# Performance work log

Measured on AMD Instinct MI355X. Metric: run time of the kernel, lower is better.

Reference implementation:

```python
import jax, jax.numpy as jnp
import numpy as np

N_HEAD = 16


def setup_inputs() -> dict:
    key = jax.random.key(0)
    k1, k2, k3 = jax.random.split(key, 3)
    B, T, C = 4, 2048, 2048
    x = jax.random.normal(k1, (B, T, C), dtype=jnp.float32)
    # weights stored as [in, out] so y = x @ W + b (equivalent to torch Linear)
    w_attn = jax.random.normal(k2, (C, 3 * C), dtype=jnp.float32) * 0.02
    b_attn = jnp.zeros((3 * C,), dtype=jnp.float32)
    w_proj = jax.random.normal(k3, (C, C), dtype=jnp.float32) * 0.02
    b_proj = jnp.zeros((C,), dtype=jnp.float32)
    return {"x": x, "w_attn": w_attn, "b_attn": b_attn, "w_proj": w_proj, "b_proj": b_proj}


def reference(x, w_attn, b_attn, w_proj, b_proj):
    B, T, C = x.shape
    H = N_HEAD
    D = C // H
    qkv = x @ w_attn + b_attn                     # [B,T,3C]
    q, k, v = jnp.split(qkv, 3, axis=-1)
    q = q.reshape(B, T, H, D).transpose(0, 2, 1, 3)  # [B,H,T,D]
    k = k.reshape(B, T, H, D).transpose(0, 2, 1, 3)
    v = v.reshape(B, T, H, D).transpose(0, 2, 1, 3)
    att = jnp.einsum("bhqd,bhkd->bhqk", q, k) * (1.0 / jnp.sqrt(jnp.float32(D)))
    causal = jnp.tril(jnp.ones((T, T), dtype=bool))
    att = jnp.where(causal[None, None], att, jnp.float32(-jnp.inf))
    att = jax.nn.softmax(att, axis=-1)
    y = jnp.einsum("bhqk,bhkd->bhqd", att, v)     # [B,H,T,D]
    y = y.transpose(0, 2, 1, 3).reshape(B, T, C)
    return y @ w_proj + b_proj
```

## Files before the change

### kernel.cpp

```cpp
#include <hip/hip_runtime.h>
#include <cstdint>

typedef unsigned short u16;
typedef u16   u16x4 __attribute__((ext_vector_type(4)));
typedef u16   u16x8 __attribute__((ext_vector_type(8)));
typedef short s16x8 __attribute__((ext_vector_type(8)));
typedef float f32x4 __attribute__((ext_vector_type(4)));

__device__ __forceinline__ u16 f2bf(float f) {
  union { float f; unsigned u; } v; v.f = f;
  unsigned u = v.u;
  return (u16)((u + 0x7fffu + ((u >> 16) & 1u)) >> 16);
}

__device__ __forceinline__ void gld_lds16(const u16* g, u16* l) {
  __builtin_amdgcn_global_load_lds((const __attribute__((address_space(1))) void*)g,
                                   (__attribute__((address_space(3))) void*)l, 16, 0, 0);
}

__device__ __forceinline__ void transpose_cast_body(
    const float* __restrict__ in, u16* __restrict__ outp, int R, int Cin,
    int cx, int cy, u16 (*tile)[72]) {
  const int c0 = cx * 64, r0 = cy * 64;
  const int t = threadIdx.x;
  const int r = t >> 2, cs = (t & 3) * 16;
  const float* src = in + (size_t)(r0 + r) * Cin + c0 + cs;
#pragma unroll
  for (int q = 0; q < 4; ++q) {
    float4 v = *(const float4*)(src + q * 4);
    tile[r][cs + q * 4 + 0] = f2bf(v.x);
    tile[r][cs + q * 4 + 1] = f2bf(v.y);
    tile[r][cs + q * 4 + 2] = f2bf(v.z);
    tile[r][cs + q * 4 + 3] = f2bf(v.w);
  }
  __syncthreads();
  u16x8 w0, w1;
#pragma unroll
  for (int q = 0; q < 8; ++q) { w0[q] = tile[cs + q][r]; w1[q] = tile[cs + 8 + q][r]; }
  u16* dst = outp + (size_t)(c0 + r) * R + r0 + cs;
  *(u16x8*)dst = w0;
  *(u16x8*)(dst + 8) = w1;
}

__global__ void prep_k(const float* __restrict__ x, u16* __restrict__ xb,
                       const float* __restrict__ w_attn, u16* __restrict__ waT,
                       const float* __restrict__ w_proj, u16* __restrict__ wpT) {
  __shared__ u16 tile[64][72];
  const int bx = blockIdx.x;
  if (bx < 8192) {
    size_t i = ((size_t)bx * 256 + threadIdx.x) * 8;
    float4 a = *(const float4*)(x + i);
    float4 b = *(const float4*)(x + i + 4);
    u16x8 r;
    r[0] = f2bf(a.x); r[1] = f2bf(a.y); r[2] = f2bf(a.z); r[3] = f2bf(a.w);
    r[4] = f2bf(b.x); r[5] = f2bf(b.y); r[6] = f2bf(b.z); r[7] = f2bf(b.w);
    *(u16x8*)(xb + i) = r;
  } else if (bx < 11264) {
    int idx = bx - 8192;
    transpose_cast_body(w_attn, waT, 2048, 6144, idx % 96, idx / 96, tile);
  } else {
    int idx = bx - 11264;
    transpose_cast_body(w_proj, wpT, 2048, 2048, idx % 32, idx / 32, tile);
  }
}

template <int EPI>
__global__ __launch_bounds__(512, 2) void gemm256(
    const u16* __restrict__ A, const u16* __restrict__ Bt,
    const float* __restrict__ bias,
    u16* __restrict__ o0, u16* __restrict__ o1, u16* __restrict__ o2,
    float* __restrict__ ofp, int Ntiles, int Kdim) {
  __shared__ __align__(128) u16 sm[65536];
  const int nwg = gridDim.x;
  const int orig = blockIdx.x;
  const int qq = nwg >> 3;
  const int bid = (orig & 7) * qq + (orig >> 3);
  const int mt = bid / Ntiles, nt = bid % Ntiles;
  const int tid = threadIdx.x, lane = tid & 63, wave = tid >> 6;
  const int wr = wave >> 2, wc = wave & 3;
  const int l15 = lane & 15, lhi = lane >> 4;
  f32x4 acc[8][4] = {};
  const int nK = Kdim >> 6;

#define VMA(n) asm volatile("s_waitcnt vmcnt(" #n ")" ::: "memory")
#define BARK   asm volatile("s_barrier" ::: "memory")
#define DSA(qm)                                                                          \
  do {                                                                                   \
    _Pragma("unroll") for (int mi = 0; mi < 4; ++mi)                                     \
    _Pragma("unroll") for (int kk = 0; kk < 2; ++kk)                                     \
      af[mi * 2 + kk] = *(const s16x8*)&sm[(size_t)(cA + (qm) * 1024 +                   \
          (kk * 4 + lhi) * 128 + wr * 64 + mi * 16 + l15) * 8];                          \
  } while (0)
#define DSB(dst, qn)                                                                     \
  do {                                                                                   \
    _Pragma("unroll") for (int ni = 0; ni < 2; ++ni)                                     \
    _Pragma("unroll") for (int kk = 0; kk < 2; ++kk)                                     \
      dst[ni * 2 + kk] = *(const s16x8*)&sm[(size_t)(cB + (qn) * 1024 +                  \
          (kk * 4 + lhi) * 128 + wc * 32 + ni * 16 + l15) * 8];                          \
  } while (0)
#define STA(qm, k0, sbase)                                                               \
  do {                                                                                   \
    _Pragma("unroll") for (int l = 0; l < 2; ++l)                                        \
      gld_lds16(A + (size_t)(mt * 256 + (wave & 1) * 128 + (qm) * 64 + lane) * Kdim +    \
                    (k0) + (l * 4 + (wave >> 1)) * 8,                                    \
                &sm[(size_t)((sbase) + (qm) * 1024 + l * 512 + wave * 64) * 8]);         \
  } while (0)
#define STB(qn, k0, sbase)                                                               \
  do {                                                                                   \
    _Pragma("unroll") for (int l = 0; l < 2; ++l)                                        \
      gld_lds16(Bt + (size_t)(nt * 256 + ((wave & 1) * 2 + (lane >> 5)) * 64 +           \
                              (qn) * 32 + (lane & 31)) * Kdim +                          \
                     (k0) + (l * 4 + (wave >> 1)) * 8,                                   \
                &sm[(size_t)((sbase) + (qn) * 1024 + l * 512 + wave * 64) * 8]);         \
  } while (0)
#define MM(qm, qn, BF)                                                                   \
  do {                                                                                   \
    __builtin_amdgcn_s_setprio(1);                                                       \
    _Pragma("unroll") for (int mi = 0; mi < 4; ++mi)                                     \
    _Pragma("unroll") for (int ni = 0; ni < 2; ++ni)                                     \
    _Pragma("unroll") for (int kk = 0; kk < 2; ++kk)                                     \
      acc[(qm) * 4 + mi][(qn) * 2 + ni] = __builtin_amdgcn_mfma_f32_16x16x32_bf16(       \
          af[mi * 2 + kk], BF[ni * 2 + kk], acc[(qm) * 4 + mi][(qn) * 2 + ni], 0, 0, 0); \
    __builtin_amdgcn_s_setprio(0);                                                       \
  } while (0)

  STA(0, 0, 0); STB(0, 0, 4096); STB(1, 0, 4096); STA(1, 0, 0);
  VMA(4);
  BARK;

  for (int t = 0; t < nK; ++t) {
    const int cA = (t & 1) * 2048, cB = 4096 + (t & 1) * 2048;
    const int sA = ((t & 1) ^ 1) * 2048, sB = 4096 + ((t & 1) ^ 1) * 2048;
    const int k1 = (t + 1) << 6;
    const bool st = (t + 1 < nK);
    s16x8 af[8], bf0[4], bf1[4];
    DSA(0); DSB(bf0, 0);
    if (st) { STA(0, k1, sA); VMA(4); } else { VMA(2); }
    BARK; MM(0, 0, bf0); BARK;
    DSB(bf1, 1);
    if (st) { STB(0, k1, sB); VMA(4); } else { VMA(0); }
    BARK; MM(0, 1, bf1); BARK;
    DSA(1);
    if (st) STB(1, k1, sB);
    BARK; MM(1, 1, bf1); BARK;
    if (st) { STA(1, k1, sA); VMA(4); }
    BARK; MM(1, 0, bf0); BARK;
  }
#undef VMA
#undef BARK
#undef DSA
#undef DSB
#undef STA
#undef STB
#undef MM

  const int row0 = mt * 256 + wr * 128;
  const int col0 = nt * 256 + wc * 64;
  float bcol[4];
#pragma unroll
  for (int ni = 0; ni < 4; ++ni) bcol[ni] = bias[col0 + ni * 16 + l15];
  if constexpr (EPI == 0) {
#pragma unroll
    for (int ni = 0; ni < 4; ++ni) {
      int cc = col0 + ni * 16 + l15;
      int which = cc >> 11, h = (cc >> 7) & 15, d = cc & 127;
      if (which == 2) {
#pragma unroll
        for (int mi = 0; mi < 8; ++mi) {
          int t0 = row0 + mi * 16 + lhi * 4;
          int bb = t0 >> 11, tt = t0 & 2047;
          u16x4 w;
#pragma unroll
          for (int j = 0; j < 4; ++j) w[j] = f2bf(acc[mi][ni][j] + bcol[ni]);
          *(u16x4*)&o2[(((size_t)bb * 16 + h) * 128 + d) * 2048 + tt] = w;
        }
      } else {
        u16* o = (which == 0) ? o0 : o1;
#pragma unroll
        for (int mi = 0; mi < 8; ++mi)
#pragma unroll
          for (int j = 0; j < 4; ++j) {
            int row = row0 + mi * 16 + lhi * 4 + j;
            int bb = row >> 11, tt = row & 2047;
            o[(((size_t)bb * 16 + h) * 2048 + tt) * 128 + d] = f2bf(acc[mi][ni][j] + bcol[ni]);
          }
      }
    }
  } else {
#pragma unroll
    for (int mi = 0; mi < 8; ++mi)
#pragma unroll
      for (int j = 0; j < 4; ++j) {
        int row = row0 + mi * 16 + lhi * 4 + j;
#pragma unroll
        for (int ni = 0; ni < 4; ++ni)
          ofp[(size_t)row * 2048 + col0 + ni * 16 + l15] = acc[mi][ni][j] + bcol[ni];
      }
  }
}

__global__ __launch_bounds__(512, 4) void attn_k(
    const u16* __restrict__ Q, const u16* __restrict__ Kg,
    const u16* __restrict__ Vt, u16* __restrict__ Y) {
  __shared__ u16 Ks[8192];
  __shared__ u16 Vs[8192];
  __shared__ u16 Ps[8][16 * 72];
  const int p = blockIdx.x, bh = blockIdx.y;
  const int tid = threadIdx.x, lane = tid & 63, wave = tid >> 6;
  const int l15 = lane & 15, lhi = lane >> 4;
  const size_t bhT = (size_t)bh * 2048;
  const int b = bh >> 4, h = bh & 15;
  const float sc = 0.08838834764831845f * 1.4426950408889634f;

  for (int hf = 0; hf < 2; ++hf) {
    const int qt = hf ? 15 - p : p;
    const int r0 = qt * 128 + wave * 16;
    const int last = 2 * qt + 1;

    s16x8 qf[4];
#pragma unroll
    for (int kk = 0; kk < 4; ++kk)
      qf[kk] = *(const s16x8*)&Q[(bhT + r0 + l15) * 128 + kk * 32 + lhi * 8];

    f32x4 o[8] = {};
    float m_[4], l_[4];
#pragma unroll
    for (int j = 0; j < 4; ++j) { m_[j] = -1e30f; l_[j] = 0.f; }

    __syncthreads();
#pragma unroll
    for (int c = 0; c < 2; ++c) {
      int ci = c * 512 + tid;
      int dhi = ci >> 6, key = ci & 63;
      gld_lds16(Kg + (bhT + key) * 128 + dhi * 8, &Ks[(c * 512 + wave * 64) * 8]);
      int khi = ci >> 7, d = ci & 127;
      gld_lds16(Vt + ((size_t)bh * 128 + d) * 2048 + khi * 8, &Vs[(c * 512 + wave * 64) * 8]);
    }
    __syncthreads();

    for (int it = 0; it <= last; ++it) {
      const int j0 = it * 64;
      const bool have_next = (it < last);
      u16x8 kpre[2], vpre[2];
      if (have_next) {
        const int j1 = j0 + 64;
#pragma unroll
        for (int c = 0; c < 2; ++c) {
          int ci = c * 512 + tid;
          int dhi = ci >> 6, key = ci & 63;
          kpre[c] = *(const u16x8*)&Kg[(bhT + j1 + key) * 128 + dhi * 8];
          int khi = ci >> 7, d = ci & 127;
          vpre[c] = *(const u16x8*)&Vt[((size_t)bh * 128 + d) * 2048 + j1 + khi * 8];
        }
      }

      if (j0 <= r0 + 15) {
        f32x4 s[4] = {};
#pragma unroll
        for (int nc = 0; nc < 4; ++nc)
#pragma unroll
          for (int kk = 0; kk < 4; ++kk) {
            s16x8 kf = *(const s16x8*)&Ks[((kk * 4 + lhi) * 64 + nc * 16 + l15) * 8];
            s[nc] = __builtin_amdgcn_mfma_f32_16x16x32_bf16(qf[kk], kf, s[nc], 0, 0, 0);
          }
        const bool maskt = (j0 + 63 > r0);
        float rmax[4];
#pragma unroll
        for (int j = 0; j < 4; ++j) rmax[j] = -1e30f;
#pragma unroll
        for (int nc = 0; nc < 4; ++nc)
#pragma unroll
          for (int j = 0; j < 4; ++j) {
            float v = s[nc][j] * sc;
            if (maskt && (j0 + nc * 16 + l15) > (r0 + lhi * 4 + j)) v = -1e30f;
            s[nc][j] = v;
            rmax[j] = fmaxf(rmax[j], v);
          }
#pragma unroll
        for (int off = 1; off < 16; off <<= 1)
#pragma unroll
          for (int j = 0; j < 4; ++j) rmax[j] = fmaxf(rmax[j], __shfl_xor(rmax[j], off));

        float al[4], rsum[4];
#pragma unroll
        for (int j = 0; j < 4; ++j) {
          float mn = fmaxf(m_[j], rmax[j]);
          al[j] = exp2f(m_[j] - mn);
          m_[j] = mn;
          rsum[j] = 0.f;
        }
#pragma unroll
        for (int nc = 0; nc < 4; ++nc)
#pragma unroll
          for (int j = 0; j < 4; ++j) {
            float pv = exp2f(s[nc][j] - m_[j]);
            rsum[j] += pv;
            Ps[wave][(lhi * 4 + j) * 72 + nc * 16 + l15] = f2bf(pv);
          }
#pragma unroll
        for (int off = 1; off < 16; off <<= 1)
#pragma unroll
          for (int j = 0; j < 4; ++j) rsum[j] += __shfl_xor(rsum[j], off);
#pragma unroll
        for (int j = 0; j < 4; ++j) l_[j] = l_[j] * al[j] + rsum[j];
#pragma unroll
        for (int di = 0; di < 8; ++di)
#pragma unroll
          for (int j = 0; j < 4; ++j) o[di][j] *= al[j];

#pragma unroll
        for (int kk2 = 0; kk2 < 2; ++kk2) {
          s16x8 pf = *(const s16x8*)&Ps[wave][l15 * 72 + kk2 * 32 + lhi * 8];
#pragma unroll
          for (int di = 0; di < 8; ++di) {
            s16x8 vf = *(const s16x8*)&Vs[((kk2 * 4 + lhi) * 128 + di * 16 + l15) * 8];
            o[di] = __builtin_amdgcn_mfma_f32_16x16x32_bf16(pf, vf, o[di], 0, 0, 0);
          }
        }
      }

      if (have_next) {
        __syncthreads();
#pragma unroll
        for (int c = 0; c < 2; ++c) {
          *(u16x8*)&Ks[(c * 512 + tid) * 8] = kpre[c];
          *(u16x8*)&Vs[(c * 512 + tid) * 8] = vpre[c];
        }
        __syncthreads();
      }
    }

    float rl[4];
#pragma unroll
    for (int j = 0; j < 4; ++j) rl[j] = 1.0f / l_[j];
#pragma unroll
    for (int di = 0; di < 8; ++di)
#pragma unroll
      for (int j = 0; j < 4; ++j) {
        int row = b * 2048 + r0 + lhi * 4 + j;
        int col = h * 128 + di * 16 + l15;
        Y[(size_t)row * 2048 + col] = f2bf(o[di][j] * rl[j]);
      }
  }
}

extern "C" void kernel_launch(void* const* d_in, const int* in_sizes, int n_in,
                              void* d_out, int out_size, void* d_ws, size_t ws_size,
                              hipStream_t stream) {
  const float* x      = (const float*)d_in[0];
  const float* w_attn = (const float*)d_in[1];
  const float* b_attn = (const float*)d_in[2];
  const float* w_proj = (const float*)d_in[3];
  const float* b_proj = (const float*)d_in[4];
  float* out = (float*)d_out;

  char* ws = (char*)d_ws;
  u16* xb  = (u16*)(ws);
  u16* waT = (u16*)(ws + 33554432ull);
  u16* wpT = (u16*)(ws + 58720256ull);
  u16* Qb  = (u16*)(ws + 67108864ull);
  u16* Kb  = (u16*)(ws + 100663296ull);
  u16* Vtb = (u16*)(ws + 167772160ull);
  u16* Yb  = xb;

  prep_k<<<12288, 256, 0, stream>>>(x, xb, w_attn, waT, w_proj, wpT);
  gemm256<0><<<32 * 24, 512, 0, stream>>>(xb, waT, b_attn, Qb, Kb, Vtb, nullptr, 24, 2048);
  attn_k<<<dim3(8, 64), 512, 0, stream>>>(Qb, Kb, Vtb, Yb);
  gemm256<1><<<32 * 8, 512, 0, stream>>>(Yb, wpT, b_proj, nullptr, nullptr, nullptr, out, 8, 2048);
}
```

Measured before the change: 554.6 us.

## Deepen GEMM global-to-LDS prefetch to two K-tiles ahead

Restructures the 256x256 GEMM main loop so global-to-LDS loads are issued up to two K steps ahead instead of one. The quarter-tile LDS slots are reused in a staggered order, and the loop is peeled into a steady state plus two epilogue iterations with adjusted vmcnt wait counts. The aim is to hide more global memory latency behind MFMA work. The cost is more outstanding loads and a tricky buffer-reuse schedule whose correctness depends on the exact wait counts.

Result: no change. 558.0 us (+0.6%).

```diff
diff --git a/kernel.cpp b/kernel.cpp
--- a/kernel.cpp
+++ b/kernel.cpp
@@ -82,7 +82,7 @@
   f32x4 acc[8][4] = {};
   const int nK = Kdim >> 6;
 
-#define VMA(n) asm volatile("s_waitcnt vmcnt(" #n ")" ::: "memory")
+#define VMA(n) asm volatile("s_waitcnt vmcnt(" n ")" ::: "memory")
 #define BARK   asm volatile("s_barrier" ::: "memory")
 #define DSA(qm)                                                                          \
   do {                                                                                   \
@@ -123,29 +123,40 @@
           af[mi * 2 + kk], BF[ni * 2 + kk], acc[(qm) * 4 + mi][(qn) * 2 + ni], 0, 0, 0); \
     __builtin_amdgcn_s_setprio(0);                                                       \
   } while (0)
+#define TILE(t, DO1, DO2, V0, V1, V3)                                                    \
+  do {                                                                                   \
+    const int cA = ((t) & 1) * 2048, cB = 4096 + ((t) & 1) * 2048;                       \
+    const int sA1 = (((t) + 1) & 1) * 2048;                                              \
+    const int sA2 = ((t) & 1) * 2048, sB2 = 4096 + ((t) & 1) * 2048;                     \
+    const int k1 = ((t) + 1) << 6, k2 = ((t) + 2) << 6;                                  \
+    s16x8 af[8], bf0[4], bf1[4];                                                         \
+                                                                                \
+    DSA(0); DSB(bf0, 0);                                                                 \
+    if (DO1) STA(1, k1, sA1);                                                            \
+    VMA(V0); BARK; MM(0, 0, bf0); BARK;                                                  \
+                                                                                \
+    DSB(bf1, 1);                                                                         \
+    if (DO2) STA(0, k2, sA2);                                                            \
+    VMA(V1); BARK; MM(0, 1, bf1); BARK;                                                  \
+                                                                                \
+    DSA(1);                                                                              \
+    if (DO2) STB(0, k2, sB2);                                                            \
+    BARK; MM(1, 1, bf1); BARK;                                                           \
+                                                                                \
+    if (DO2) STB(1, k2, sB2);                                                            \
+    if (DO1) VMA(V3);                                                                    \
+    BARK; MM(1, 0, bf0); BARK;                                                           \
+  } while (0)
 
   STA(0, 0, 0); STB(0, 0, 4096); STB(1, 0, 4096); STA(1, 0, 0);
-  VMA(4);
+  STA(0, 64, 2048); STB(0, 64, 6144); STB(1, 64, 6144);
+  VMA("10");
   BARK;
 
-  for (int t = 0; t < nK; ++t) {
-    const int cA = (t & 1) * 2048, cB = 4096 + (t & 1) * 2048;
-    const int sA = ((t & 1) ^ 1) * 2048, sB = 4096 + ((t & 1) ^ 1) * 2048;
-    const int k1 = (t + 1) << 6;
-    const bool st = (t + 1 < nK);
-    s16x8 af[8], bf0[4], bf1[4];
-    DSA(0); DSB(bf0, 0);
-    if (st) { STA(0, k1, sA); VMA(4); } else { VMA(2); }
-    BARK; MM(0, 0, bf0); BARK;
-    DSB(bf1, 1);
-    if (st) { STB(0, k1, sB); VMA(4); } else { VMA(0); }
-    BARK; MM(0, 1, bf1); BARK;
-    DSA(1);
-    if (st) STB(1, k1, sB);
-    BARK; MM(1, 1, bf1); BARK;
-    if (st) { STA(1, k1, sA); VMA(4); }
-    BARK; MM(1, 0, bf0); BARK;
-  }
+  for (int t = 0; t < nK - 2; ++t) TILE(t, true, true, "10", "10", "10");
+  TILE(nK - 2, true, false, "10", "8", "4");
+  TILE(nK - 1, false, false, "2", "0", "0");
+
 #undef VMA
 #undef BARK
 #undef DSA
@@ -153,6 +164,7 @@
 #undef STA
 #undef STB
 #undef MM
+#undef TILE
 
   const int row0 = mt * 256 + wr * 128;
   const int col0 = nt * 256 + wc * 64;
```

## Restructure GEMM to 256x128 tiles with K=32 triple-buffered LDS pipeline

Applied to the files above, without the earlier changes.

Rewrites the GEMM kernel. The output tile shrinks from 256x256 to 256x128 and the K step from 64 to 32. Shared memory drops to about 72KB, so launch bounds can request 4 blocks per CU, and loads run through a 3-stage ring buffer with one barrier per K step instead of the earlier quadrant schedule with many barriers. The aim is more occupancy, more blocks (the last GEMM goes from 256 to 512 blocks, enough to fill the CUs) and less sync overhead. The cost is lower arithmetic intensity per tile and more global and LDS traffic, which could offset the gains.

Result: slower. 813.4 us (+46.7%).

```diff
diff --git a/kernel.cpp b/kernel.cpp
--- a/kernel.cpp
+++ b/kernel.cpp
@@ -65,97 +65,74 @@
 }
 
 template <int EPI>
-__global__ __launch_bounds__(512, 2) void gemm256(
+__global__ __launch_bounds__(512, 4) void gemm256(
     const u16* __restrict__ A, const u16* __restrict__ Bt,
     const float* __restrict__ bias,
     u16* __restrict__ o0, u16* __restrict__ o1, u16* __restrict__ o2,
     float* __restrict__ ofp, int Ntiles, int Kdim) {
-  __shared__ __align__(128) u16 sm[65536];
+  __shared__ __align__(128) u16 sm[36864];
   const int nwg = gridDim.x;
   const int orig = blockIdx.x;
   const int qq = nwg >> 3;
   const int bid = (orig & 7) * qq + (orig >> 3);
   const int mt = bid / Ntiles, nt = bid % Ntiles;
   const int tid = threadIdx.x, lane = tid & 63, wave = tid >> 6;
-  const int wr = wave >> 2, wc = wave & 3;
+  const int wr = wave >> 1, wc = wave & 1;
   const int l15 = lane & 15, lhi = lane >> 4;
-  f32x4 acc[8][4] = {};
-  const int nK = Kdim >> 6;
-
-#define VMA(n) asm volatile("s_waitcnt vmcnt(" #n ")" ::: "memory")
+  f32x4 acc[4][4] = {};
+  const int nK = Kdim >> 5;
+
+#define VMA(n) asm volatile("s_waitcnt vmcnt(" n ")" ::: "memory")
 #define BARK   asm volatile("s_barrier" ::: "memory")
-#define DSA(qm)                                                                          \
-  do {                                                                                   \
-    _Pragma("unroll") for (int mi = 0; mi < 4; ++mi)                                     \
-    _Pragma("unroll") for (int kk = 0; kk < 2; ++kk)                                     \
-      af[mi * 2 + kk] = *(const s16x8*)&sm[(size_t)(cA + (qm) * 1024 +                   \
-          (kk * 4 + lhi) * 128 + wr * 64 + mi * 16 + l15) * 8];                          \
+#define STAGE(t)                                                                  \
+  do {                                                                            \
+    const int sl_ = (t) % 3;                                                      \
+    const int k0_ = (t) << 5;                                                     \
+    _Pragma("unroll") for (int j = 0; j < 2; ++j) {                               \
+      int ci = j * 512 + tid;                                                     \
+      int row = ci & 255, khi = ci >> 8;                                          \
+      gld_lds16(A + (size_t)(mt * 256 + row) * Kdim + k0_ + khi * 8,              \
+                &sm[(size_t)(sl_ * 1024 + ci) * 8]);                              \
+    }                                                                             \
+    {                                                                             \
+      int row = tid & 127, khi = tid >> 7;                                        \
+      gld_lds16(Bt + (size_t)(nt * 128 + row) * Kdim + k0_ + khi * 8,             \
+                &sm[(size_t)(3072 + sl_ * 512 + tid) * 8]);                       \
+    }                                                                             \
   } while (0)
-#define DSB(dst, qn)                                                                     \
-  do {                                                                                   \
-    _Pragma("unroll") for (int ni = 0; ni < 2; ++ni)                                     \
-    _Pragma("unroll") for (int kk = 0; kk < 2; ++kk)                                     \
-      dst[ni * 2 + kk] = *(const s16x8*)&sm[(size_t)(cB + (qn) * 1024 +                  \
-          (kk * 4 + lhi) * 128 + wc * 32 + ni * 16 + l15) * 8];                          \
+#define TILE(t, VN, DOS)                                                          \
+  do {                                                                            \
+    VMA(VN);                                                                      \
+    BARK;                                                                         \
+    const int cs_ = (t) % 3;                                                      \
+    s16x8 af[4], bf[4];                                                           \
+    _Pragma("unroll") for (int mi = 0; mi < 4; ++mi)                              \
+      af[mi] = *(const s16x8*)&sm[(size_t)(cs_ * 1024 + lhi * 256 +               \
+          wr * 64 + mi * 16 + l15) * 8];                                          \
+    _Pragma("unroll") for (int ni = 0; ni < 4; ++ni)                              \
+      bf[ni] = *(const s16x8*)&sm[(size_t)(3072 + cs_ * 512 + lhi * 128 +         \
+          wc * 64 + ni * 16 + l15) * 8];                                          \
+    if (DOS) STAGE((t) + 2);                                                      \
+    __builtin_amdgcn_s_setprio(1);                                                \
+    _Pragma("unroll") for (int mi = 0; mi < 4; ++mi)                              \
+    _Pragma("unroll") for (int ni = 0; ni < 4; ++ni)                              \
+      acc[mi][ni] = __builtin_amdgcn_mfma_f32_16x16x32_bf16(                      \
+          af[mi], bf[ni], acc[mi][ni], 0, 0, 0);                                  \
+    __builtin_amdgcn_s_setprio(0);                                                \
   } while (0)
-#define STA(qm, k0, sbase)                                                               \
-  do {                                                                                   \
-    _Pragma("unroll") for (int l = 0; l < 2; ++l)                                        \
-      gld_lds16(A + (size_t)(mt * 256 + (wave & 1) * 128 + (qm) * 64 + lane) * Kdim +    \
-                    (k0) + (l * 4 + (wave >> 1)) * 8,                                    \
-                &sm[(size_t)((sbase) + (qm) * 1024 + l * 512 + wave * 64) * 8]);         \
-  } while (0)
-#define STB(qn, k0, sbase)                                                               \
-  do {                                                                                   \
-    _Pragma("unroll") for (int l = 0; l < 2; ++l)                                        \
-      gld_lds16(Bt + (size_t)(nt * 256 + ((wave & 1) * 2 + (lane >> 5)) * 64 +           \
-                              (qn) * 32 + (lane & 31)) * Kdim +                          \
-                     (k0) + (l * 4 + (wave >> 1)) * 8,                                   \
-                &sm[(size_t)((sbase) + (qn) * 1024 + l * 512 + wave * 64) * 8]);         \
-  } while (0)
-#define MM(qm, qn, BF)                                                                   \
-  do {                                                                                   \
-    __builtin_amdgcn_s_setprio(1);                                                       \
-    _Pragma("unroll") for (int mi = 0; mi < 4; ++mi)                                     \
-    _Pragma("unroll") for (int ni = 0; ni < 2; ++ni)                                     \
-    _Pragma("unroll") for (int kk = 0; kk < 2; ++kk)                                     \
-      acc[(qm) * 4 + mi][(qn) * 2 + ni] = __builtin_amdgcn_mfma_f32_16x16x32_bf16(       \
-          af[mi * 2 + kk], BF[ni * 2 + kk], acc[(qm) * 4 + mi][(qn) * 2 + ni], 0, 0, 0); \
-    __builtin_amdgcn_s_setprio(0);                                                       \
-  } while (0)
-
-  STA(0, 0, 0); STB(0, 0, 4096); STB(1, 0, 4096); STA(1, 0, 0);
-  VMA(4);
-  BARK;
-
-  for (int t = 0; t < nK; ++t) {
-    const int cA = (t & 1) * 2048, cB = 4096 + (t & 1) * 2048;
-    const int sA = ((t & 1) ^ 1) * 2048, sB = 4096 + ((t & 1) ^ 1) * 2048;
-    const int k1 = (t + 1) << 6;
-    const bool st = (t + 1 < nK);
-    s16x8 af[8], bf0[4], bf1[4];
-    DSA(0); DSB(bf0, 0);
-    if (st) { STA(0, k1, sA); VMA(4); } else { VMA(2); }
-    BARK; MM(0, 0, bf0); BARK;
-    DSB(bf1, 1);
-    if (st) { STB(0, k1, sB); VMA(4); } else { VMA(0); }
-    BARK; MM(0, 1, bf1); BARK;
-    DSA(1);
-    if (st) STB(1, k1, sB);
-    BARK; MM(1, 1, bf1); BARK;
-    if (st) { STA(1, k1, sA); VMA(4); }
-    BARK; MM(1, 0, bf0); BARK;
-  }
+
+  STAGE(0); STAGE(1);
+  for (int t = 0; t < nK - 2; ++t) TILE(t, "3", true);
+  TILE(nK - 2, "3", false);
+  TILE(nK - 1, "0", false);
+
 #undef VMA
 #undef BARK
-#undef DSA
-#undef DSB
-#undef STA
-#undef STB
-#undef MM
-
-  const int row0 = mt * 256 + wr * 128;
-  const int col0 = nt * 256 + wc * 64;
+#undef STAGE
+#undef TILE
+
+  const int row0 = mt * 256 + wr * 64;
+  const int col0 = nt * 128 + wc * 64;
   float bcol[4];
 #pragma unroll
   for (int ni = 0; ni < 4; ++ni) bcol[ni] = bias[col0 + ni * 16 + l15];
@@ -166,7 +143,7 @@
       int which = cc >> 11, h = (cc >> 7) & 15, d = cc & 127;
       if (which == 2) {
 #pragma unroll
-        for (int mi = 0; mi < 8; ++mi) {
+        for (int mi = 0; mi < 4; ++mi) {
           int t0 = row0 + mi * 16 + lhi * 4;
           int bb = t0 >> 11, tt = t0 & 2047;
           u16x4 w;
@@ -177,7 +154,7 @@
       } else {
         u16* o = (which == 0) ? o0 : o1;
 #pragma unroll
-        for (int mi = 0; mi < 8; ++mi)
+        for (int mi = 0; mi < 4; ++mi)
 #pragma unroll
           for (int j = 0; j < 4; ++j) {
             int row = row0 + mi * 16 + lhi * 4 + j;
@@ -188,7 +165,7 @@
     }
   } else {
 #pragma unroll
-    for (int mi = 0; mi < 8; ++mi)
+    for (int mi = 0; mi < 4; ++mi)
 #pragma unroll
       for (int j = 0; j < 4; ++j) {
         int row = row0 + mi * 16 + lhi * 4 + j;
@@ -364,7 +341,7 @@
   u16* Yb  = xb;
 
   prep_k<<<12288, 256, 0, stream>>>(x, xb, w_attn, waT, w_proj, wpT);
-  gemm256<0><<<32 * 24, 512, 0, stream>>>(xb, waT, b_attn, Qb, Kb, Vtb, nullptr, 24, 2048);
+  gemm256<0><<<32 * 48, 512, 0, stream>>>(xb, waT, b_attn, Qb, Kb, Vtb, nullptr, 48, 2048);
   attn_k<<<dim3(8, 64), 512, 0, stream>>>(Qb, Kb, Vtb, Yb);
-  gemm256<1><<<32 * 8, 512, 0, stream>>>(Yb, wpT, b_proj, nullptr, nullptr, nullptr, out, 8, 2048);
-}
+  gemm256<1><<<32 * 16, 512, 0, stream>>>(Yb, wpT, b_proj, nullptr, nullptr, nullptr, out, 16, 2048);
+}
```
